# Kernel tuning notes

Hardware: AMD Instinct MI355X
Metric: run time of the kernel (lower is better)

Reference implementation:

```python
import jax, jax.numpy as jnp
import numpy as np

N_SRC = 100000
N_DST = 20000
E = 640000
IN_FEATS = 256
NUM_HEADS = 4
OUT_FEATS = 32
NEG_SLOPE = 0.2


def setup_inputs() -> dict:
    key = jax.random.key(0)
    ks = jax.random.split(key, 8)
    x = jax.random.normal(ks[0], (N_SRC, IN_FEATS), dtype=jnp.float32)
    src_idx = jax.random.randint(ks[1], (E,), 0, N_SRC)
    dst_idx = jax.random.randint(ks[2], (E,), 0, N_DST)
    dst_to_src = jax.random.randint(ks[3], (N_DST,), 0, N_SRC)
    # parameters (xavier-ish scale)
    W = jax.random.normal(ks[4], (IN_FEATS, NUM_HEADS * OUT_FEATS), dtype=jnp.float32) * (1.0 / np.sqrt(IN_FEATS))
    attn_l = jax.random.normal(ks[5], (NUM_HEADS, OUT_FEATS), dtype=jnp.float32) * 0.1
    attn_r = jax.random.normal(ks[6], (NUM_HEADS, OUT_FEATS), dtype=jnp.float32) * 0.1
    return {"x": x, "W": W, "attn_l": attn_l, "attn_r": attn_r,
            "src_idx": src_idx, "dst_idx": dst_idx, "dst_to_src": dst_to_src}


def reference(x, W, attn_l, attn_r, src_idx, dst_idx, dst_to_src):
    # fc + reshape to heads: [N_src, H, D]
    h = (x @ W).reshape(N_SRC, NUM_HEADS, OUT_FEATS)
    # per-src-node left attention score: [N_src, H]
    el = jnp.einsum('nhd,hd->nh', h, attn_l)
    # self_gather: dst nodes are a subset of src nodes
    h_dst = h[dst_to_src]                       # [N_dst, H, D]
    er = jnp.einsum('nhd,hd->nh', h_dst, attn_r)  # [N_dst, H]
    # apply_edge + leaky_relu: per-edge scores [E, H]
    e = el[src_idx] + er[dst_idx]
    e = jnp.where(e >= 0, e, NEG_SLOPE * e)
    # NOTE: original code normalizes leaky_relu(e) directly (no exp)
    sum_e = jax.ops.segment_sum(e, dst_idx, num_segments=N_DST)  # [N_dst, H]
    attention = e / sum_e[dst_idx]              # [E, H]
    # attention_gather: weighted scatter-add of src features to dst
    msg = attention[:, :, None] * h[src_idx]    # [E, H, D]
    out = jax.ops.segment_sum(msg, dst_idx, num_segments=N_DST)  # [N_dst, H, D]
    return out
```

## Files before the change

### kernel.cpp

```cpp
#include <hip/hip_runtime.h>

#define N_SRC 100000
#define N_DST 20000
#define NE 640000
#define IN_F 256
#define NH 4
#define DF 32
#define NCOL 128

__global__ void k_prep(const float* __restrict__ W,
                       const float* __restrict__ attn_l,
                       const float* __restrict__ attn_r,
                       double* __restrict__ Wlr_t) {
    int k = threadIdx.x;
    for (int j = 0; j < 8; ++j) {
        const float* attn = (j < 4) ? attn_l : attn_r;
        int hh = j & 3;
        double s = 0.0;
        for (int d = 0; d < DF; ++d)
            s += (double)W[k * NCOL + hh * DF + d] * (double)attn[hh * DF + d];
        Wlr_t[(size_t)j * IN_F + k] = s;
    }
}

__global__ __launch_bounds__(256) void k_gemm(const float* __restrict__ x,
                                              const float* __restrict__ W,
                                              const double* __restrict__ Wlr_t,
                                              const int* __restrict__ dst_idx,
                                              float* __restrict__ h,
                                              double* __restrict__ el,
                                              double* __restrict__ er_src,
                                              int* __restrict__ cnt) {
    __shared__ float xs[32][68];
    __shared__ double wlds[8][66];
    const int tid = threadIdx.x;
    const int row0 = blockIdx.x * 32;
    const int c0 = (tid & 31) * 4;
    const int r0 = (tid >> 5) * 4;
    const int srow = tid >> 3;
    const int sj = tid & 7;

    float acc[4][4];
#pragma unroll
    for (int j = 0; j < 4; ++j)
#pragma unroll
        for (int m = 0; m < 4; ++m) acc[j][m] = 0.f;
    double sacc = 0.0;

    for (int chunk = 0; chunk < 4; ++chunk) {
        const int kbase = chunk * 64;
        if (chunk) __syncthreads();
#pragma unroll
        for (int t = 0; t < 2; ++t) {
            int i = t * 256 + tid;
            int r = i >> 4;
            int q = i & 15;
            *((float4*)&xs[r][q * 4]) =
                *((const float4*)(x + (size_t)(row0 + r) * IN_F + kbase + q * 4));
        }
#pragma unroll
        for (int t = 0; t < 2; ++t) {
            int i = t * 256 + tid;
            int j = i >> 6;
            int k = i & 63;
            wlds[j][k] = Wlr_t[(size_t)j * IN_F + kbase + k];
        }
        __syncthreads();

#pragma unroll 4
        for (int kq = 0; kq < 64; kq += 4) {
            const float* wp = W + (size_t)(kbase + kq) * NCOL + c0;
            float4 w0 = *((const float4*)(wp));
            float4 w1 = *((const float4*)(wp + NCOL));
            float4 w2 = *((const float4*)(wp + 2 * NCOL));
            float4 w3 = *((const float4*)(wp + 3 * NCOL));
#pragma unroll
            for (int j = 0; j < 4; ++j) {
                float4 xv = *((const float4*)&xs[r0 + j][kq]);
                acc[j][0] += xv.x * w0.x + xv.y * w1.x + xv.z * w2.x + xv.w * w3.x;
                acc[j][1] += xv.x * w0.y + xv.y * w1.y + xv.z * w2.y + xv.w * w3.y;
                acc[j][2] += xv.x * w0.z + xv.y * w1.z + xv.z * w2.z + xv.w * w3.z;
                acc[j][3] += xv.x * w0.w + xv.y * w1.w + xv.z * w2.w + xv.w * w3.w;
            }
        }

        {
#pragma unroll 4
            for (int k = 0; k < 64; k += 4) {
                float4 xv = *((const float4*)&xs[srow][k]);
                double2 wa = *((const double2*)&wlds[sj][k]);
                double2 wb = *((const double2*)&wlds[sj][k + 2]);
                sacc += (double)xv.x * wa.x + (double)xv.y * wa.y
                      + (double)xv.z * wb.x + (double)xv.w * wb.y;
            }
        }
    }

#pragma unroll
    for (int j = 0; j < 4; ++j) {
        int row = row0 + r0 + j;
        *((float4*)(h + (size_t)row * NCOL + c0)) =
            make_float4(acc[j][0], acc[j][1], acc[j][2], acc[j][3]);
    }

    {
        int row = row0 + srow;
        if (sj < 4) el[(size_t)row * NH + sj] = sacc;
        else        er_src[(size_t)row * NH + (sj - 4)] = sacc;
    }

    for (int e = blockIdx.x * 256 + tid; e < NE; e += gridDim.x * 256)
        atomicAdd(cnt + dst_idx[e], 1);
}

__global__ __launch_bounds__(1024) void k_scan(const int* __restrict__ cnt,
                                               int* __restrict__ offsets,
                                               int* __restrict__ cursor) {
    __shared__ int wsum[16];
    __shared__ int carry;
    int tid = threadIdx.x, lane = tid & 63, w = tid >> 6;
    if (tid == 0) carry = 0;
    __syncthreads();
    for (int base = 0; base < N_DST; base += 1024) {
        int i = base + tid;
        int v = (i < N_DST) ? cnt[i] : 0;
        int s = v;
#pragma unroll
        for (int off = 1; off < 64; off <<= 1) {
            int t = __shfl_up(s, off);
            if (lane >= off) s += t;
        }
        if (lane == 63) wsum[w] = s;
        __syncthreads();
        int wprefix = 0;
        for (int k = 0; k < w; ++k) wprefix += wsum[k];
        int incl = s + wprefix + carry;
        if (i < N_DST) {
            offsets[i + 1] = incl;
            cursor[i] = 0;
        }
        __syncthreads();
        if (tid == 1023) carry = incl;
        __syncthreads();
    }
    if (tid == 0) offsets[0] = 0;
}

__global__ __launch_bounds__(256) void k_fill(const int* __restrict__ src_idx,
                                              const int* __restrict__ dst_idx,
                                              const int* __restrict__ offsets,
                                              int* __restrict__ cursor,
                                              int* __restrict__ edge_src) {
    int gid = blockIdx.x * 256 + threadIdx.x;
    if (gid >= NE) return;
    int d = dst_idx[gid];
    int pos = offsets[d] + atomicAdd(cursor + d, 1);
    edge_src[pos] = src_idx[gid];
}

__global__ __launch_bounds__(256) void k_fused(const int* __restrict__ offsets,
                                               const int* __restrict__ edge_src,
                                               const double* __restrict__ el,
                                               const double* __restrict__ er_src,
                                               const int* __restrict__ dst_to_src,
                                               const float* __restrict__ h,
                                               float* __restrict__ out) {
    __shared__ double att_sh[4][4][68];
    __shared__ int    s_sh[4][64];

    const int w = threadIdx.x >> 6;
    const int lane = threadIdx.x & 63;
    const int d = blockIdx.x * 4 + w;
    if (d >= N_DST) return;
    const int beg = offsets[d];
    const int deg = offsets[d + 1] - beg;

    const int srcd = dst_to_src[d];
    double2 era = *((const double2*)(er_src + (size_t)srcd * NH));
    double2 erb = *((const double2*)(er_src + (size_t)srcd * NH + 2));
    const double er0 = era.x, er1 = era.y, er2 = erb.x, er3 = erb.y;

    double sum0 = 0.0, sum1 = 0.0, sum2 = 0.0, sum3 = 0.0;
    double e0r = 0.0, e1r = 0.0, e2r = 0.0, e3r = 0.0;
    int s_first = 0;
    for (int j = lane; j < deg; j += 64) {
        int s = edge_src[beg + j];
        double2 ela = *((const double2*)(el + (size_t)s * NH));
        double2 elb = *((const double2*)(el + (size_t)s * NH + 2));
        double e0 = ela.x + er0; e0 = (e0 >= 0.0) ? e0 : 0.2 * e0;
        double e1 = ela.y + er1; e1 = (e1 >= 0.0) ? e1 : 0.2 * e1;
        double e2 = elb.x + er2; e2 = (e2 >= 0.0) ? e2 : 0.2 * e2;
        double e3 = elb.y + er3; e3 = (e3 >= 0.0) ? e3 : 0.2 * e3;
        sum0 += e0; sum1 += e1; sum2 += e2; sum3 += e3;
        if (j == lane) { s_first = s; e0r = e0; e1r = e1; e2r = e2; e3r = e3; }
    }
#pragma unroll
    for (int m = 32; m >= 1; m >>= 1) {
        sum0 += __shfl_xor(sum0, m);
        sum1 += __shfl_xor(sum1, m);
        sum2 += __shfl_xor(sum2, m);
        sum3 += __shfl_xor(sum3, m);
    }

    if (lane < deg) {
        s_sh[w][lane] = s_first;
        att_sh[w][0][lane] = e0r / sum0;
        att_sh[w][1][lane] = e1r / sum1;
        att_sh[w][2][lane] = e2r / sum2;
        att_sh[w][3][lane] = e3r / sum3;
    }

    const int js = lane >> 5;
    const int cq = lane & 31;
    const int hd = cq >> 3;
    const double Shd = (hd == 0) ? sum0 : (hd == 1) ? sum1 : (hd == 2) ? sum2 : sum3;
    const double erhd = (hd == 0) ? er0 : (hd == 1) ? er1 : (hd == 2) ? er2 : er3;

    double acc0 = 0.0, acc1 = 0.0, acc2 = 0.0, acc3 = 0.0;
    for (int j = js; j < deg; j += 2) {
        int s; double att;
        if (j < 64) {
            s = s_sh[w][j];
            att = att_sh[w][hd][j];
        } else {
            s = edge_src[beg + j];
            double e = el[(size_t)s * NH + hd] + erhd;
            e = (e >= 0.0) ? e : 0.2 * e;
            att = e / Shd;
        }
        float4 hv = *((const float4*)(h + (size_t)s * NCOL + cq * 4));
        acc0 += att * (double)hv.x;
        acc1 += att * (double)hv.y;
        acc2 += att * (double)hv.z;
        acc3 += att * (double)hv.w;
    }
    acc0 += __shfl_xor(acc0, 32);
    acc1 += __shfl_xor(acc1, 32);
    acc2 += __shfl_xor(acc2, 32);
    acc3 += __shfl_xor(acc3, 32);

    if (lane < 32) {
        *((float4*)(out + (size_t)d * NCOL + lane * 4)) =
            make_float4((float)acc0, (float)acc1, (float)acc2, (float)acc3);
    }
}

extern "C" void kernel_launch(void* const* d_in, const int* in_sizes, int n_in,
                              void* d_out, int out_size, void* d_ws, size_t ws_size,
                              hipStream_t stream) {
    const float* x      = (const float*)d_in[0];
    const float* W      = (const float*)d_in[1];
    const float* attn_l = (const float*)d_in[2];
    const float* attn_r = (const float*)d_in[3];
    const int* src_idx  = (const int*)d_in[4];
    const int* dst_idx  = (const int*)d_in[5];
    const int* dst_to_src = (const int*)d_in[6];
    float* out = (float*)d_out;

    char* p = (char*)d_ws;
    double* Wlr_t  = (double*)p;  p += (size_t)8 * IN_F * sizeof(double);
    double* el     = (double*)p;  p += (size_t)N_SRC * NH * sizeof(double);
    double* er_src = (double*)p;  p += (size_t)N_SRC * NH * sizeof(double);
    float*  h      = (float*)p;   p += (size_t)N_SRC * NCOL * sizeof(float);
    int*    cnt      = (int*)p;   p += (size_t)N_DST * sizeof(int);
    int*    offsets  = (int*)p;   p += (size_t)(N_DST + 1) * sizeof(int);
    int*    cursor   = (int*)p;   p += (size_t)N_DST * sizeof(int);
    int*    edge_src = (int*)p;   p += (size_t)NE * sizeof(int);

    hipMemsetAsync(cnt, 0, (size_t)N_DST * sizeof(int), stream);

    k_prep<<<1, 256, 0, stream>>>(W, attn_l, attn_r, Wlr_t);
    k_gemm<<<N_SRC / 32, 256, 0, stream>>>(x, W, Wlr_t, dst_idx, h, el, er_src, cnt);
    k_scan<<<1, 1024, 0, stream>>>(cnt, offsets, cursor);
    k_fill<<<(NE + 255) / 256, 256, 0, stream>>>(src_idx, dst_idx, offsets, cursor, edge_src);
    k_fused<<<N_DST / 4, 256, 0, stream>>>(offsets, edge_src, el, er_src, dst_to_src, h, out);
}
```

Baseline: 279.8 us.

## Compute er only for dst nodes and prefetch next GEMM chunk into registers

```diff
diff --git a/kernel.cpp b/kernel.cpp
--- a/kernel.cpp
+++ b/kernel.cpp
@@ -29,16 +29,20 @@
                                               const int* __restrict__ dst_idx,
                                               float* __restrict__ h,
                                               double* __restrict__ el,
-                                              double* __restrict__ er_src,
                                               int* __restrict__ cnt) {
     __shared__ float xs[32][68];
-    __shared__ double wlds[8][66];
+    __shared__ double wlds[4][66];
     const int tid = threadIdx.x;
     const int row0 = blockIdx.x * 32;
     const int c0 = (tid & 31) * 4;
     const int r0 = (tid >> 5) * 4;
     const int srow = tid >> 3;
-    const int sj = tid & 7;
+    const int shh = tid & 3;
+    const int shalf = (tid >> 2) & 1;
+
+    const int sr0 = tid >> 4,          sq0 = (tid & 15) * 4;
+    const int sr1 = (256 + tid) >> 4,  sq1 = (tid & 15) * 4;
+    const int wj = tid >> 6, wk = tid & 63;
 
     float acc[4][4];
 #pragma unroll
@@ -46,26 +50,25 @@
 #pragma unroll
         for (int m = 0; m < 4; ++m) acc[j][m] = 0.f;
     double sacc = 0.0;
+
+    float4 pf0 = *((const float4*)(x + (size_t)(row0 + sr0) * IN_F + sq0));
+    float4 pf1 = *((const float4*)(x + (size_t)(row0 + sr1) * IN_F + sq1));
+    double pfw = Wlr_t[(size_t)wj * IN_F + wk];
 
     for (int chunk = 0; chunk < 4; ++chunk) {
         const int kbase = chunk * 64;
         if (chunk) __syncthreads();
-#pragma unroll
-        for (int t = 0; t < 2; ++t) {
-            int i = t * 256 + tid;
-            int r = i >> 4;
-            int q = i & 15;
-            *((float4*)&xs[r][q * 4]) =
-                *((const float4*)(x + (size_t)(row0 + r) * IN_F + kbase + q * 4));
-        }
-#pragma unroll
-        for (int t = 0; t < 2; ++t) {
-            int i = t * 256 + tid;
-            int j = i >> 6;
-            int k = i & 63;
-            wlds[j][k] = Wlr_t[(size_t)j * IN_F + kbase + k];
-        }
+        *((float4*)&xs[sr0][sq0]) = pf0;
+        *((float4*)&xs[sr1][sq1]) = pf1;
+        wlds[wj][wk] = pfw;
         __syncthreads();
+
+        if (chunk < 3) {
+            const int nk = kbase + 64;
+            pf0 = *((const float4*)(x + (size_t)(row0 + sr0) * IN_F + nk + sq0));
+            pf1 = *((const float4*)(x + (size_t)(row0 + sr1) * IN_F + nk + sq1));
+            pfw = Wlr_t[(size_t)wj * IN_F + nk + wk];
+        }
 
 #pragma unroll 4
         for (int kq = 0; kq < 64; kq += 4) {
@@ -85,11 +88,12 @@
         }
 
         {
+            const int kb = shalf * 32;
 #pragma unroll 4
-            for (int k = 0; k < 64; k += 4) {
-                float4 xv = *((const float4*)&xs[srow][k]);
-                double2 wa = *((const double2*)&wlds[sj][k]);
-                double2 wb = *((const double2*)&wlds[sj][k + 2]);
+            for (int k = 0; k < 32; k += 4) {
+                float4 xv = *((const float4*)&xs[srow][kb + k]);
+                double2 wa = *((const double2*)&wlds[shh][kb + k]);
+                double2 wb = *((const double2*)&wlds[shh][kb + k + 2]);
                 sacc += (double)xv.x * wa.x + (double)xv.y * wa.y
                       + (double)xv.z * wb.x + (double)xv.w * wb.y;
             }
@@ -103,14 +107,41 @@
             make_float4(acc[j][0], acc[j][1], acc[j][2], acc[j][3]);
     }
 
-    {
-        int row = row0 + srow;
-        if (sj < 4) el[(size_t)row * NH + sj] = sacc;
-        else        er_src[(size_t)row * NH + (sj - 4)] = sacc;
-    }
+    sacc += __shfl_xor(sacc, 4);
+    if (shalf == 0)
+        el[(size_t)(row0 + srow) * NH + shh] = sacc;
 
     for (int e = blockIdx.x * 256 + tid; e < NE; e += gridDim.x * 256)
         atomicAdd(cnt + dst_idx[e], 1);
+}
+
+__global__ __launch_bounds__(256) void k_er(const float* __restrict__ x,
+                                            const double* __restrict__ Wlr_t,
+                                            const int* __restrict__ dst_to_src,
+                                            double* __restrict__ er_dst) {
+    const int lane = threadIdx.x & 63;
+    const int d = blockIdx.x * 4 + (threadIdx.x >> 6);
+    if (d >= N_DST) return;
+    const int srcrow = dst_to_src[d];
+    float4 xv = *((const float4*)(x + (size_t)srcrow * IN_F + lane * 4));
+    const double xd[4] = {(double)xv.x, (double)xv.y, (double)xv.z, (double)xv.w};
+    double acc[4];
+#pragma unroll
+    for (int hh = 0; hh < 4; ++hh) {
+        const double* wp = Wlr_t + (size_t)(4 + hh) * IN_F + lane * 4;
+        acc[hh] = xd[0] * wp[0] + xd[1] * wp[1] + xd[2] * wp[2] + xd[3] * wp[3];
+    }
+#pragma unroll
+    for (int hh = 0; hh < 4; ++hh) {
+#pragma unroll
+        for (int m = 32; m >= 1; m >>= 1)
+            acc[hh] += __shfl_xor(acc[hh], m);
+    }
+    if (lane == 0) {
+        double2* o = (double2*)(er_dst + (size_t)d * NH);
+        o[0] = make_double2(acc[0], acc[1]);
+        o[1] = make_double2(acc[2], acc[3]);
+    }
 }
 
 __global__ __launch_bounds__(1024) void k_scan(const int* __restrict__ cnt,
@@ -161,8 +192,7 @@
 __global__ __launch_bounds__(256) void k_fused(const int* __restrict__ offsets,
                                                const int* __restrict__ edge_src,
                                                const double* __restrict__ el,
-                                               const double* __restrict__ er_src,
-                                               const int* __restrict__ dst_to_src,
+                                               const double* __restrict__ er_dst,
                                                const float* __restrict__ h,
                                                float* __restrict__ out) {
     __shared__ double att_sh[4][4][68];
@@ -175,9 +205,8 @@
     const int beg = offsets[d];
     const int deg = offsets[d + 1] - beg;
 
-    const int srcd = dst_to_src[d];
-    double2 era = *((const double2*)(er_src + (size_t)srcd * NH));
-    double2 erb = *((const double2*)(er_src + (size_t)srcd * NH + 2));
+    double2 era = *((const double2*)(er_dst + (size_t)d * NH));
+    double2 erb = *((const double2*)(er_dst + (size_t)d * NH + 2));
     const double er0 = era.x, er1 = era.y, er2 = erb.x, er3 = erb.y;
 
     double sum0 = 0.0, sum1 = 0.0, sum2 = 0.0, sum3 = 0.0;
@@ -260,7 +289,7 @@
     char* p = (char*)d_ws;
     double* Wlr_t  = (double*)p;  p += (size_t)8 * IN_F * sizeof(double);
     double* el     = (double*)p;  p += (size_t)N_SRC * NH * sizeof(double);
-    double* er_src = (double*)p;  p += (size_t)N_SRC * NH * sizeof(double);
+    double* er_dst = (double*)p;  p += (size_t)N_DST * NH * sizeof(double);
     float*  h      = (float*)p;   p += (size_t)N_SRC * NCOL * sizeof(float);
     int*    cnt      = (int*)p;   p += (size_t)N_DST * sizeof(int);
     int*    offsets  = (int*)p;   p += (size_t)(N_DST + 1) * sizeof(int);
@@ -270,8 +299,9 @@
     hipMemsetAsync(cnt, 0, (size_t)N_DST * sizeof(int), stream);
 
     k_prep<<<1, 256, 0, stream>>>(W, attn_l, attn_r, Wlr_t);
-    k_gemm<<<N_SRC / 32, 256, 0, stream>>>(x, W, Wlr_t, dst_idx, h, el, er_src, cnt);
+    k_gemm<<<N_SRC / 32, 256, 0, stream>>>(x, W, Wlr_t, dst_idx, h, el, cnt);
+    k_er<<<N_DST / 4, 256, 0, stream>>>(x, Wlr_t, dst_to_src, er_dst);
     k_scan<<<1, 1024, 0, stream>>>(cnt, offsets, cursor);
     k_fill<<<(NE + 255) / 256, 256, 0, stream>>>(src_idx, dst_idx, offsets, cursor, edge_src);
-    k_fused<<<N_DST / 4, 256, 0, stream>>>(offsets, edge_src, el, er_src, dst_to_src, h, out);
-}
+    k_fused<<<N_DST / 4, 256, 0, stream>>>(offsets, edge_src, el, er_dst, h, out);
+}
```

Result: no change. 283.5 us (+1.3%).
